# Performance work log

Measured on AMD Instinct MI355X. Metric: run time of the kernel, lower is better.

## Reference

```python
import jax, jax.numpy as jnp
import numpy as np

B, STREAM, IN_CH = 128, 512, 4
EXTRA, GROUPS, DEPTH = 5, 2, 3
STEP, LENGTH = 16, 32
RNN, OUT = 256, 10
C = IN_CH + 1 + EXTRA              # augmented channels: original + time + 1x1-conv
SIG_C = C + C * C + C ** 3          # signature channels per group at depth 3
W = (STREAM - LENGTH) // STEP + 1   # number of sliding windows = GRU steps
F = GROUPS * SIG_C                  # GRU input features


def _outer(a, b):
    # flattened tensor (outer) product on last axis: (...,m),(...,n)->(...,m*n)
    return (a[..., :, None] * b[..., None, :]).reshape(a.shape[:-1] + (a.shape[-1] * b.shape[-1],))


def _chen_step(S, dx):
    # Chen's identity: S <- S (tensor) exp(dx). S is a tuple of flattened
    # signature levels (..., C^k), k=1..DEPTH; dx has shape (..., C).
    P = [jnp.ones(dx.shape[:-1] + (1,), dx.dtype)]  # dx^{(x)j}/j!, j=0..DEPTH
    for j in range(1, DEPTH + 1):
        P.append(_outer(P[-1], dx) / j)
    newS = []
    for k in range(1, DEPTH + 1):
        acc = P[k]  # S_0 (x) P_k
        for j in range(k):
            acc = acc + _outer(S[k - 1 - j], P[j])
        newS.append(acc)
    return tuple(newS)


def setup_inputs() -> dict:
    key = jax.random.key(0)
    ks = jax.random.split(key, 10)
    s_aug = 1.0 / np.sqrt(IN_CH)
    s_rnn = 1.0 / np.sqrt(RNN)
    return {
        "x": jax.random.normal(ks[0], (B, STREAM, IN_CH), jnp.float32),
        "W_aug": jax.random.uniform(ks[1], (GROUPS, EXTRA, IN_CH), jnp.float32, -s_aug, s_aug),
        "b_aug": jax.random.uniform(ks[2], (GROUPS, EXTRA), jnp.float32, -s_aug, s_aug),
        "W_ih": jax.random.uniform(ks[3], (3 * RNN, F), jnp.float32, -s_rnn, s_rnn),
        "W_hh": jax.random.uniform(ks[4], (3 * RNN, RNN), jnp.float32, -s_rnn, s_rnn),
        "b_ih": jax.random.uniform(ks[5], (3 * RNN,), jnp.float32, -s_rnn, s_rnn),
        "b_hh": jax.random.uniform(ks[6], (3 * RNN,), jnp.float32, -s_rnn, s_rnn),
        "W_out": jax.random.uniform(ks[7], (OUT, RNN), jnp.float32, -s_rnn, s_rnn),
        "b_out": jax.random.uniform(ks[8], (OUT,), jnp.float32, -s_rnn, s_rnn),
    }


def reference(x, W_aug, b_aug, W_ih, W_hh, b_ih, b_hh, W_out, b_out):
    # (a) linear augmentation per channel group: [original | time | conv1x1(x)]
    t = jnp.linspace(0.0, 1.0, STREAM, dtype=x.dtype)
    t = jnp.broadcast_to(t[None, :, None], (B, STREAM, 1))
    aug = jnp.einsum('bsi,gei->bgse', x, W_aug) + b_aug[None, :, None, :]  # (B,G,S,EXTRA)
    base = jnp.broadcast_to(jnp.concatenate([x, t], -1)[:, None],
                            (B, GROUPS, STREAM, IN_CH + 1))
    xa = jnp.concatenate([base, aug], -1)            # (B,G,S,C)
    xa = xa.reshape(B * GROUPS, STREAM, C)

    # (b) depth-3 signatures over sliding windows via Chen's identity
    dx = xa[:, 1:] - xa[:, :-1]                       # (BG, S-1, C)
    widx = jnp.arange(W)[:, None] * STEP + jnp.arange(LENGTH - 1)[None, :]
    dxw = dx[:, widx]                                 # (BG, W, L-1, C)
    dxw = jnp.moveaxis(dxw, 2, 0)                     # (L-1, BG, W, C)
    S0 = tuple(jnp.zeros((B * GROUPS, W, C ** k), x.dtype) for k in range(1, DEPTH + 1))
    S, _ = jax.lax.scan(lambda S, d: (_chen_step(S, d), None), S0, dxw)
    sig = jnp.concatenate(S, -1)                      # (BG, W, SIG_C)
    sig = sig.reshape(B, GROUPS, W, SIG_C)
    sig = jnp.moveaxis(sig, 2, 0).reshape(W, B, F)    # (W, B, G*SIG_C)

    # (c) GRU over window signatures (torch.nn.GRUCell math, gate order r,z,n)
    def gru(h, xt):
        gi = xt @ W_ih.T + b_ih
        gh = h @ W_hh.T + b_hh
        ir, iz, inn = jnp.split(gi, 3, -1)
        hr, hz, hn = jnp.split(gh, 3, -1)
        r = jax.nn.sigmoid(ir + hr)
        z = jax.nn.sigmoid(iz + hz)
        n = jnp.tanh(inn + r * hn)
        return (1 - z) * n + z * h, None

    h, _ = jax.lax.scan(gru, jnp.zeros((B, RNN), x.dtype), sig)
    return jax.nn.sigmoid(h @ W_out.T + b_out)        # (B, OUT)
```

## Files before the change

kernel.cpp:

```cpp
#include <hip/hip_runtime.h>
#include <hip/hip_bf16.h>
#include <stdint.h>


typedef _Float16 f16;
typedef f16  f16x2 __attribute__((ext_vector_type(2)));
typedef f16  f16x4 __attribute__((ext_vector_type(4)));
typedef f16  f16x8 __attribute__((ext_vector_type(8)));
typedef float f32x2 __attribute__((ext_vector_type(2)));
typedef float f32x4 __attribute__((ext_vector_type(4)));
typedef float f32x8 __attribute__((ext_vector_type(8)));

#define ASYNC16(gp, lp) __builtin_amdgcn_global_load_lds( \
    (const __attribute__((address_space(1))) void*)(gp),  \
    (__attribute__((address_space(3))) void*)(lp), 16, 0, 0)

#define BAR_LDS() do { asm volatile("s_waitcnt lgkmcnt(0)" ::: "memory"); \
                       __builtin_amdgcn_s_barrier();                      \
                       asm volatile("" ::: "memory"); } while (0)

__device__ __forceinline__ float fexp2(float x) {
    float r; asm("v_exp_f32 %0, %1" : "=v"(r) : "v"(x)); return r;
}
__device__ __forceinline__ float frcp(float x) {
    float r; asm("v_rcp_f32 %0, %1" : "=v"(r) : "v"(x)); return r;
}

__global__ __launch_bounds__(256) void prep_kernel(const float* __restrict__ x,
                                                   const float* __restrict__ W_aug,
                                                   const float* __restrict__ Wih,
                                                   const float* __restrict__ Whh,
                                                   f16* __restrict__ sig16,
                                                   f16* __restrict__ wih16,
                                                   f16* __restrict__ whh16,
                                                   uint8_t* __restrict__ whh8) {
    __shared__ float dxs[4][31][10];
    __shared__ f16 srow[4][1112];
    const int tid = threadIdx.x;
    if (blockIdx.x < 840) {
        int c = blockIdx.x * 256 + tid;
        int r = c / 280, kc = (c - r * 280) * 8;
        const float* src = Wih + (size_t)r * 2220 + kc;
        f16x8 o;
        if (kc + 8 <= 2220) {
            float4 v0 = *(const float4*)(src);
            float4 v1 = *(const float4*)(src + 4);
            o[0]=(f16)v0.x; o[1]=(f16)v0.y; o[2]=(f16)v0.z; o[3]=(f16)v0.w;
            o[4]=(f16)v1.x; o[5]=(f16)v1.y; o[6]=(f16)v1.z; o[7]=(f16)v1.w;
        } else {
#pragma unroll
            for (int j = 0; j < 8; j++)
                o[j] = (f16)((kc + j < 2220) ? src[j] : 0.0f);
        }
        *(f16x8*)(wih16 + (size_t)r * 2240 + kc) = o;
        return;
    }
    if (blockIdx.x < 936) {
        int c2 = ((int)blockIdx.x - 840) * 256 + tid;
        int j8 = c2 * 8;
        float w[8];
        {
            float4 v0 = *(const float4*)(Whh + j8);
            float4 v1 = *(const float4*)(Whh + j8 + 4);
            w[0]=v0.x; w[1]=v0.y; w[2]=v0.z; w[3]=v0.w;
            w[4]=v1.x; w[5]=v1.y; w[6]=v1.z; w[7]=v1.w;
        }
        f16x8 o;
#pragma unroll
        for (int j = 0; j < 8; j++) o[j] = (f16)w[j];
        *(f16x8*)(whh16 + j8) = o;
        {
            uint32_t p01 = (uint32_t)__builtin_amdgcn_cvt_pk_fp8_f32(w[0]*16.f, w[1]*16.f, 0, false) & 0xffffu;
            uint32_t p23 = (uint32_t)__builtin_amdgcn_cvt_pk_fp8_f32(w[2]*16.f, w[3]*16.f, 0, false) & 0xffffu;
            uint32_t p45 = (uint32_t)__builtin_amdgcn_cvt_pk_fp8_f32(w[4]*16.f, w[5]*16.f, 0, false) & 0xffffu;
            uint32_t p67 = (uint32_t)__builtin_amdgcn_cvt_pk_fp8_f32(w[6]*16.f, w[7]*16.f, 0, false) & 0xffffu;
            uint2 st = make_uint2(p01 | (p23 << 16), p45 | (p67 << 16));
            *(uint2*)(whh8 + j8) = st;
        }
        return;
    }
    const int sub = tid >> 6, t64 = tid & 63;
    const int cid = ((int)blockIdx.x - 936) * 4 + sub;
    const int w = cid % 31;
    const int bg = cid / 31;
    const int b = bg >> 1, g = bg & 1;
    if (t64 < 31) {
        int s = w * 16 + t64;
        const float4 x0 = *(const float4*)(x + ((size_t)b * 512 + s) * 4);
        const float4 x1 = *(const float4*)(x + ((size_t)b * 512 + s + 1) * 4);
        float d0 = x1.x - x0.x, d1 = x1.y - x0.y, d2 = x1.z - x0.z, d3 = x1.w - x0.w;
        dxs[sub][t64][0] = d0; dxs[sub][t64][1] = d1;
        dxs[sub][t64][2] = d2; dxs[sub][t64][3] = d3;
        dxs[sub][t64][4] = 1.0f / 511.0f;
#pragma unroll
        for (int e = 0; e < 5; e++) {
            const float* wa = W_aug + (g * 5 + e) * 4;
            dxs[sub][t64][5 + e] = d0 * wa[0] + d1 * wa[1] + d2 * wa[2] + d3 * wa[3];
        }
    }
    __syncthreads();
    size_t base = ((size_t)(w * 128 + b)) * 2240 + (size_t)g * 1110;
    if (t64 < 50) {
        int p0 = 2 * t64, p1 = p0 + 1;
        int i0 = p0 / 10, j0 = p0 % 10, j1 = j0 + 1;
        const float* dz  = &dxs[sub][0][0];
        const float* pI  = dz + i0;
        const float* pJ0 = dz + j0;
        const float* pJ1 = dz + j1;
        float s3a[10], s3b[10];
#pragma unroll
        for (int k = 0; k < 10; k++) { s3a[k] = 0.f; s3b[k] = 0.f; }
        float s2a = 0.f, s2b = 0.f, s1 = 0.f;
        for (int l = 0; l < 31; l++) {
            const float* row = dz + l * 10;
            float di  = pI[l * 10];
            float dj0 = pJ0[l * 10];
            float dj1 = pJ1[l * 10];
            float t0 = s1 + di * (1.0f / 3.0f);
            float a0 = s2a + t0 * (0.5f * dj0);
            float a1 = s2b + t0 * (0.5f * dj1);
#pragma unroll
            for (int k = 0; k < 10; k++) {
                float dk = row[k];
                s3a[k] += a0 * dk;
                s3b[k] += a1 * dk;
            }
            float u = s1 + 0.5f * di;
            s2a += u * dj0;
            s2b += u * dj1;
            s1 += di;
        }
        *(f16x2*)&srow[sub][10 + p0] = (f16x2){(f16)s2a, (f16)s2b};
#pragma unroll
        for (int k = 0; k < 5; k++)
            *(f16x2*)&srow[sub][110 + p0 * 10 + 2 * k] =
                (f16x2){(f16)s3a[2 * k], (f16)s3a[2 * k + 1]};
#pragma unroll
        for (int k = 0; k < 5; k++)
            *(f16x2*)&srow[sub][110 + p1 * 10 + 2 * k] =
                (f16x2){(f16)s3b[2 * k], (f16)s3b[2 * k + 1]};
    } else if (t64 < 60) {
        int c = t64 - 50;
        const float* pc = &dxs[sub][0][0] + c;
        float s = 0.f;
        for (int l = 0; l < 31; l++) s += pc[l * 10];
        srow[sub][c] = (f16)s;
    }
    __syncthreads();
    for (int j = t64; j < 555; j += 64)
        *(f16x2*)(sig16 + base + 2 * j) = *(const f16x2*)&srow[sub][2 * j];
    if (g == 1 && t64 < 10)
        *(f16x2*)(sig16 + ((size_t)(w * 128 + b)) * 2240 + 2220 + 2 * t64) =
            (f16x2){(f16)0.0f, (f16)0.0f};
}

__global__ __launch_bounds__(512) void gemm_kernel(const f16* __restrict__ A,
                                                   const f16* __restrict__ Bw,
                                                   const float* __restrict__ bias,
                                                   const float* __restrict__ bhh,
                                                   f16* __restrict__ Cgi) {
    const int lin = blockIdx.x;
    const int nc = lin % 12;
    const int mb = lin / 12;
    const int t = mb >> 1, half = mb & 1;
    __shared__ __align__(16) f16 As[2][3][64 * 32];
    __shared__ __align__(16) f16 Bs[2][3][64 * 32];
    __shared__ __align__(16) float sc[4][16 * 64];
    const int tid = threadIdx.x, lane = tid & 63, wid = tid >> 6;
    const int kh = wid >> 2, w4 = wid & 3;
    const int l16 = lane & 15, quad = lane >> 4;
    const int lrow = lane >> 2, lk = lane & 3;
    const int Nbase = nc * 64;
    const f16* gaA = A  + (size_t)(mb * 64 + w4 * 16 + lrow) * 2240 + kh * 1120 + lk * 8;
    const f16* gbB = Bw + (size_t)(Nbase + w4 * 16 + lrow) * 2240 + kh * 1120 + lk * 8;

#define GISSUE(KT, BUF) do { \
        int _k0 = (KT) * 32; \
        ASYNC16(gaA + _k0, &As[kh][BUF][(w4 * 16) * 32]); \
        ASYNC16(gbB + _k0, &Bs[kh][BUF][(w4 * 16) * 32]); } while (0)

#define GCOMPUTE(BUF) do { \
        f16x8 af, bf[4]; \
        af = *(const f16x8*)&As[kh][BUF][(w4 * 16 + l16) * 32 + quad * 8]; \
        _Pragma("unroll") \
        for (int nt = 0; nt < 4; nt++) \
            bf[nt] = *(const f16x8*)&Bs[kh][BUF][(nt * 16 + l16) * 32 + quad * 8]; \
        _Pragma("unroll") \
        for (int nt = 0; nt < 4; nt++) \
            acc[nt] = __builtin_amdgcn_mfma_f32_16x16x32_f16(af, bf[nt], acc[nt], 0, 0, 0); } while (0)

    f32x4 acc[4];
#pragma unroll
    for (int nt = 0; nt < 4; nt++) acc[nt] = (f32x4){0.f, 0.f, 0.f, 0.f};

    GISSUE(0, 0); GISSUE(1, 1);
    for (int kt = 0; kt < 33; kt++) {
        asm volatile("s_waitcnt vmcnt(2) lgkmcnt(0)\n\ts_barrier" ::: "memory");
        GISSUE(kt + 2, (kt + 2) % 3);
        GCOMPUTE(kt % 3);
    }
    asm volatile("s_waitcnt vmcnt(2) lgkmcnt(0)\n\ts_barrier" ::: "memory");
    GCOMPUTE(0);
    asm volatile("s_waitcnt vmcnt(0) lgkmcnt(0)\n\ts_barrier" ::: "memory");
    GCOMPUTE(1);

    if (kh == 1) {
#pragma unroll
        for (int nt = 0; nt < 4; nt++)
#pragma unroll
            for (int rr = 0; rr < 4; rr++)
                sc[w4][(quad * 4 + rr) * 64 + nt * 16 + l16] = acc[nt][rr];
    }
    __syncthreads();
    if (kh == 0) {
        const float NEG_LOG2E = -1.4426950408889634f;
        const float TWO_LOG2E =  2.8853900817779268f;
        const int bbv = half * 4 + w4;
#pragma unroll
        for (int nt = 0; nt < 4; nt++) {
            int col = Nbase + nt * 16 + l16;
            float bvv = bias[col] + (col < 512 ? bhh[col] : 0.0f);
            float scl = (col < 512) ? NEG_LOG2E : TWO_LOG2E;
            int gs = col >> 8, hcc = col & 255;
            int gw = hcc >> 5, gtc = (hcc >> 4) & 1, gl = hcc & 15;
            int u = gs * 2 + gtc;
            int gtid = gw * 64 + quad * 16 + gl;
            size_t off = ((size_t)((t * 8 + bbv) * 6 + u)) * 2048 + (size_t)gtid * 4;
            f16x4 st;
#pragma unroll
            for (int rr = 0; rr < 4; rr++) {
                float v = acc[nt][rr] + sc[w4][(quad * 4 + rr) * 64 + nt * 16 + l16];
                st[rr] = (f16)((v + bvv) * scl);
            }
            *(f16x4*)(Cgi + off) = st;
        }
    }
#undef GISSUE
#undef GCOMPUTE
}

#define ACLOB96 \
  "a0","a1","a2","a3","a4","a5","a6","a7","a8","a9","a10","a11","a12","a13","a14","a15", \
  "a16","a17","a18","a19","a20","a21","a22","a23","a24","a25","a26","a27","a28","a29","a30","a31", \
  "a32","a33","a34","a35","a36","a37","a38","a39","a40","a41","a42","a43","a44","a45","a46","a47", \
  "a48","a49","a50","a51","a52","a53","a54","a55","a56","a57","a58","a59","a60","a61","a62","a63", \
  "a64","a65","a66","a67","a68","a69","a70","a71","a72","a73","a74","a75","a76","a77","a78","a79", \
  "a80","a81","a82","a83","a84","a85","a86","a87","a88","a89","a90","a91","a92","a93","a94","a95"

#define LF8X(A0,A1,A2,A3,A4,A5,A6,A7, G, TC, KF) do { \
  const uint8_t* _p = whh8 + (size_t)((G) * 256 + wid * 32 + (TC) * 16 + l16) * 256 + (KF) * 128 + quad * 32; \
  f32x4 _t0 = *(const f32x4*)_p; \
  f32x4 _t1 = *(const f32x4*)(_p + 16); \
  asm volatile("v_accvgpr_write_b32 a" #A0 ", %0\n\t" \
               "v_accvgpr_write_b32 a" #A1 ", %1\n\t" \
               "v_accvgpr_write_b32 a" #A2 ", %2\n\t" \
               "v_accvgpr_write_b32 a" #A3 ", %3\n\t" \
               "v_accvgpr_write_b32 a" #A4 ", %4\n\t" \
               "v_accvgpr_write_b32 a" #A5 ", %5\n\t" \
               "v_accvgpr_write_b32 a" #A6 ", %6\n\t" \
               "v_accvgpr_write_b32 a" #A7 ", %7" \
               :: "v"(_t0[0]), "v"(_t0[1]), "v"(_t0[2]), "v"(_t0[3]), \
                  "v"(_t1[0]), "v"(_t1[1]), "v"(_t1[2]), "v"(_t1[3]) \
               : "a" #A0, "a" #A1, "a" #A2, "a" #A3, \
                 "a" #A4, "a" #A5, "a" #A6, "a" #A7); } while (0)

__global__ __launch_bounds__(512, 2) void gru_kernel(const f16* __restrict__ gi,
                                                     const f16* __restrict__ whh16,
                                                     const uint8_t* __restrict__ whh8,
                                                     const float* __restrict__ b_hh,
                                                     const float* __restrict__ W_out,
                                                     const float* __restrict__ b_out,
                                                     float* __restrict__ out) {
    __shared__ __align__(16) f16 hbufF[16 * 280];
    __shared__ __align__(16) uint8_t hbuf8[2][16 * 272];
    const int tid = threadIdx.x, lane = tid & 63, wid = tid >> 6;
    const int quad = lane >> 4, l16 = lane & 15;
    const int bb = blockIdx.x;

    for (int i = tid; i < 16 * 272; i += 512) hbuf8[1][i] = 0;

    LF8X(0,1,2,3,4,5,6,7,         0,0,0);
    LF8X(8,9,10,11,12,13,14,15,   0,0,1);
    LF8X(16,17,18,19,20,21,22,23, 0,1,0);
    LF8X(24,25,26,27,28,29,30,31, 0,1,1);
    LF8X(32,33,34,35,36,37,38,39, 1,0,0);
    LF8X(40,41,42,43,44,45,46,47, 1,0,1);
    LF8X(48,49,50,51,52,53,54,55, 1,1,0);
    LF8X(56,57,58,59,60,61,62,63, 1,1,1);
    LF8X(64,65,66,67,68,69,70,71, 2,0,0);
    LF8X(72,73,74,75,76,77,78,79, 2,0,1);
    LF8X(80,81,82,83,84,85,86,87, 2,1,0);
    LF8X(88,89,90,91,92,93,94,95, 2,1,1);

    const float C2 = 2.8853900817779268f;
    float bhn[2];
#pragma unroll
    for (int tc = 0; tc < 2; tc++) bhn[tc] = C2 * b_hh[512 + wid * 32 + tc * 16 + l16];
    float hm[2][4];
#pragma unroll
    for (int tc = 0; tc < 2; tc++)
#pragma unroll
        for (int rr = 0; rr < 4; rr++) hm[tc][rr] = 0.f;

    const size_t lanebase = (size_t)bb * 12288 + (size_t)tid * 4;
    f16x4 gcur[6];
#pragma unroll
    for (int u = 0; u < 6; u++)
        gcur[u] = *(const f16x4*)(gi + lanebase + u * 2048);

    const f32x4 zq = (f32x4){0.f, 0.f, 0.f, 0.f};

    BAR_LDS();

    for (int t = 0; t < 31; t++) {
        const uint8_t* hb = ((t & 1) ? hbuf8[0] : hbuf8[1]) + (size_t)l16 * 272 + quad * 32;
        f32x4 aR0, aR1, aZ0, aZ1, aN0, aN1;
        f32x4 u0 = *(const f32x4*)(hb);
        f32x4 u1 = *(const f32x4*)(hb + 16);
        f32x4 u2 = *(const f32x4*)(hb + 128);
        f32x4 u3 = *(const f32x4*)(hb + 144);
        f32x8 A0f, A1f;
        A0f[0]=u0[0]; A0f[1]=u0[1]; A0f[2]=u0[2]; A0f[3]=u0[3];
        A0f[4]=u1[0]; A0f[5]=u1[1]; A0f[6]=u1[2]; A0f[7]=u1[3];
        A1f[0]=u2[0]; A1f[1]=u2[1]; A1f[2]=u2[2]; A1f[3]=u2[3];
        A1f[4]=u3[0]; A1f[5]=u3[1]; A1f[6]=u3[2]; A1f[7]=u3[3];
        __builtin_amdgcn_s_setprio(1);
        asm volatile(
            "v_mfma_f32_16x16x128_f8f6f4 %[r0], %[A0], a[0:7],   %[zq]\n\t"
            "v_mfma_f32_16x16x128_f8f6f4 %[r1], %[A0], a[16:23], %[zq]\n\t"
            "v_mfma_f32_16x16x128_f8f6f4 %[z0], %[A0], a[32:39], %[zq]\n\t"
            "v_mfma_f32_16x16x128_f8f6f4 %[z1], %[A0], a[48:55], %[zq]\n\t"
            "v_mfma_f32_16x16x128_f8f6f4 %[n0], %[A0], a[64:71], %[zq]\n\t"
            "v_mfma_f32_16x16x128_f8f6f4 %[n1], %[A0], a[80:87], %[zq]\n\t"
            "v_mfma_f32_16x16x128_f8f6f4 %[r0], %[A1], a[8:15],  %[r0]\n\t"
            "v_mfma_f32_16x16x128_f8f6f4 %[r1], %[A1], a[24:31], %[r1]\n\t"
            "v_mfma_f32_16x16x128_f8f6f4 %[z0], %[A1], a[40:47], %[z0]\n\t"
            "v_mfma_f32_16x16x128_f8f6f4 %[z1], %[A1], a[56:63], %[z1]\n\t"
            "v_mfma_f32_16x16x128_f8f6f4 %[n0], %[A1], a[72:79], %[n0]\n\t"
            "v_mfma_f32_16x16x128_f8f6f4 %[n1], %[A1], a[88:95], %[n1]\n\t"
            "s_nop 7\n\ts_nop 7"
            : [r0]"=&v"(aR0), [r1]"=&v"(aR1), [z0]"=&v"(aZ0), [z1]"=&v"(aZ1),
              [n0]"=&v"(aN0), [n1]"=&v"(aN1)
            : [A0]"v"(A0f), [A1]"v"(A1f), [zq]"v"(zq)
            : ACLOB96);
        __builtin_amdgcn_s_setprio(0);

        uint8_t* hd8 = hbuf8[t & 1];
        const float C1N16 = -0.09016844005556021f;
        const float C2_16 =  0.18033688011112042f;
#pragma unroll
        for (int tc = 0; tc < 2; tc++) {
            const int hcx = wid * 32 + tc * 16 + l16;
            const f32x4 vR = tc ? aR1 : aR0;
            const f32x4 vZ = tc ? aZ1 : aZ0;
            const f32x4 vN = tc ? aN1 : aN0;
#pragma unroll
            for (int rr = 0; rr < 4; rr++) {
                float rg = frcp(1.f + fexp2(fmaf(C1N16, vR[rr], (float)gcur[tc][rr])));
                float zg = frcp(1.f + fexp2(fmaf(C1N16, vZ[rr], (float)gcur[2 + tc][rr])));
                float t2 = fmaf(rg, fmaf(C2_16, vN[rr], bhn[tc]), (float)gcur[4 + tc][rr]);
                float e2 = fexp2(t2);
                float ng = fmaf(-2.f, frcp(e2 + 1.f), 1.f);
                float h  = fmaf(zg, hm[tc][rr] - ng, ng);
                hm[tc][rr] = h;
                int pk = __builtin_amdgcn_cvt_pk_fp8_f32(h, h, 0, false);
                hd8[(quad * 4 + rr) * 272 + hcx] = (uint8_t)pk;
                if (t == 30)
                    hbufF[(quad * 4 + rr) * 280 + hcx] = (f16)h;
            }
        }
        {
            int tn = (t < 30) ? t + 1 : 30;
            const f16* gsrc = gi + (size_t)tn * 98304 + lanebase;
#pragma unroll
            for (int u = 0; u < 6; u++)
                gcur[u] = *(const f16x4*)(gsrc + u * 2048);
        }
        BAR_LDS();
    }
    if (tid < 160) {
        int r = tid / 10, oc = tid - r * 10;
        const f16* hfin = hbufF;
        float s = b_out[oc];
        for (int k = 0; k < 256; k++) s += (float)hfin[r * 280 + k] * W_out[oc * 256 + k];
        out[(bb * 16 + r) * 10 + oc] = frcp(1.f + __expf(-s));
    }
}

extern "C" void kernel_launch(void* const* d_in, const int* in_sizes, int n_in,
                              void* d_out, int out_size, void* d_ws, size_t ws_size,
                              hipStream_t stream) {
    const float* x     = (const float*)d_in[0];
    const float* W_aug = (const float*)d_in[1];
    const float* W_ih  = (const float*)d_in[3];
    const float* W_hh  = (const float*)d_in[4];
    const float* b_ih  = (const float*)d_in[5];
    const float* b_hh  = (const float*)d_in[6];
    const float* W_out = (const float*)d_in[7];
    const float* b_out = (const float*)d_in[8];
    float* out = (float*)d_out;

    char* ws = (char*)d_ws;
    const size_t SIG_BYTES  = (size_t)3968 * 2240 * 2;
    const size_t WIH_BYTES  = (size_t)768 * 2240 * 2;
    const size_t WHH_BYTES  = (size_t)768 * 256 * 2;
    const size_t WHH8_BYTES = (size_t)768 * 256;
    const size_t GI_BYTES   = (size_t)31 * 8 * 6 * 512 * 4 * 2;
    if (ws_size < SIG_BYTES + WIH_BYTES + WHH_BYTES + WHH8_BYTES + GI_BYTES) return;
    f16* sig16    = (f16*)ws;
    f16* wih16    = (f16*)(ws + SIG_BYTES);
    f16* whh16    = (f16*)(ws + SIG_BYTES + WIH_BYTES);
    uint8_t* whh8 = (uint8_t*)(ws + SIG_BYTES + WIH_BYTES + WHH_BYTES);
    f16* giw      = (f16*)(ws + SIG_BYTES + WIH_BYTES + WHH_BYTES + WHH8_BYTES);

    hipLaunchKernelGGL(prep_kernel, dim3(2920), dim3(256), 0, stream,
                       x, W_aug, W_ih, W_hh, sig16, wih16, whh16, whh8);
    hipLaunchKernelGGL(gemm_kernel, dim3(744), dim3(512), 0, stream,
                       sig16, wih16, b_ih, b_hh, giw);
    hipLaunchKernelGGL(gru_kernel, dim3(8), dim3(512), 0, stream,
                       giw, whh16, whh8, b_hh, W_out, b_out, out);
}
```

Baseline: 177.3 us.

## Split GRU hidden columns across 16 waves per block to shorten per-step chain

New measurement: 176.2 us, median of 2. Within noise of the previous version (-0.6%).

```diff
diff --git a/kernel.cpp b/kernel.cpp
--- a/kernel.cpp
+++ b/kernel.cpp
@@ -239,16 +239,13 @@
 #undef GCOMPUTE
 }
 
-#define ACLOB96 \
+#define ACLOB48 \
   "a0","a1","a2","a3","a4","a5","a6","a7","a8","a9","a10","a11","a12","a13","a14","a15", \
   "a16","a17","a18","a19","a20","a21","a22","a23","a24","a25","a26","a27","a28","a29","a30","a31", \
-  "a32","a33","a34","a35","a36","a37","a38","a39","a40","a41","a42","a43","a44","a45","a46","a47", \
-  "a48","a49","a50","a51","a52","a53","a54","a55","a56","a57","a58","a59","a60","a61","a62","a63", \
-  "a64","a65","a66","a67","a68","a69","a70","a71","a72","a73","a74","a75","a76","a77","a78","a79", \
-  "a80","a81","a82","a83","a84","a85","a86","a87","a88","a89","a90","a91","a92","a93","a94","a95"
-
-#define LF8X(A0,A1,A2,A3,A4,A5,A6,A7, G, TC, KF) do { \
-  const uint8_t* _p = whh8 + (size_t)((G) * 256 + wid * 32 + (TC) * 16 + l16) * 256 + (KF) * 128 + quad * 32; \
+  "a32","a33","a34","a35","a36","a37","a38","a39","a40","a41","a42","a43","a44","a45","a46","a47"
+
+#define LF8X(A0,A1,A2,A3,A4,A5,A6,A7, G, KF) do { \
+  const uint8_t* _p = whh8 + (size_t)((G) * 256 + wid * 16 + l16) * 256 + (KF) * 128 + quad * 32; \
   f32x4 _t0 = *(const f32x4*)_p; \
   f32x4 _t1 = *(const f32x4*)(_p + 16); \
   asm volatile("v_accvgpr_write_b32 a" #A0 ", %0\n\t" \
@@ -264,49 +261,41 @@
                : "a" #A0, "a" #A1, "a" #A2, "a" #A3, \
                  "a" #A4, "a" #A5, "a" #A6, "a" #A7); } while (0)
 
-__global__ __launch_bounds__(512, 2) void gru_kernel(const f16* __restrict__ gi,
-                                                     const f16* __restrict__ whh16,
-                                                     const uint8_t* __restrict__ whh8,
-                                                     const float* __restrict__ b_hh,
-                                                     const float* __restrict__ W_out,
-                                                     const float* __restrict__ b_out,
-                                                     float* __restrict__ out) {
+__global__ __launch_bounds__(1024, 4) void gru_kernel(const f16* __restrict__ gi,
+                                                      const f16* __restrict__ whh16,
+                                                      const uint8_t* __restrict__ whh8,
+                                                      const float* __restrict__ b_hh,
+                                                      const float* __restrict__ W_out,
+                                                      const float* __restrict__ b_out,
+                                                      float* __restrict__ out) {
     __shared__ __align__(16) f16 hbufF[16 * 280];
     __shared__ __align__(16) uint8_t hbuf8[2][16 * 272];
     const int tid = threadIdx.x, lane = tid & 63, wid = tid >> 6;
     const int quad = lane >> 4, l16 = lane & 15;
     const int bb = blockIdx.x;
 
-    for (int i = tid; i < 16 * 272; i += 512) hbuf8[1][i] = 0;
-
-    LF8X(0,1,2,3,4,5,6,7,         0,0,0);
-    LF8X(8,9,10,11,12,13,14,15,   0,0,1);
-    LF8X(16,17,18,19,20,21,22,23, 0,1,0);
-    LF8X(24,25,26,27,28,29,30,31, 0,1,1);
-    LF8X(32,33,34,35,36,37,38,39, 1,0,0);
-    LF8X(40,41,42,43,44,45,46,47, 1,0,1);
-    LF8X(48,49,50,51,52,53,54,55, 1,1,0);
-    LF8X(56,57,58,59,60,61,62,63, 1,1,1);
-    LF8X(64,65,66,67,68,69,70,71, 2,0,0);
-    LF8X(72,73,74,75,76,77,78,79, 2,0,1);
-    LF8X(80,81,82,83,84,85,86,87, 2,1,0);
-    LF8X(88,89,90,91,92,93,94,95, 2,1,1);
+    for (int i = tid; i < 16 * 272; i += 1024) hbuf8[1][i] = 0;
+
+    LF8X(0,1,2,3,4,5,6,7,         0, 0);
+    LF8X(8,9,10,11,12,13,14,15,   0, 1);
+    LF8X(16,17,18,19,20,21,22,23, 1, 0);
+    LF8X(24,25,26,27,28,29,30,31, 1, 1);
+    LF8X(32,33,34,35,36,37,38,39, 2, 0);
+    LF8X(40,41,42,43,44,45,46,47, 2, 1);
 
     const float C2 = 2.8853900817779268f;
-    float bhn[2];
-#pragma unroll
-    for (int tc = 0; tc < 2; tc++) bhn[tc] = C2 * b_hh[512 + wid * 32 + tc * 16 + l16];
-    float hm[2][4];
-#pragma unroll
-    for (int tc = 0; tc < 2; tc++)
-#pragma unroll
-        for (int rr = 0; rr < 4; rr++) hm[tc][rr] = 0.f;
-
-    const size_t lanebase = (size_t)bb * 12288 + (size_t)tid * 4;
-    f16x4 gcur[6];
-#pragma unroll
-    for (int u = 0; u < 6; u++)
-        gcur[u] = *(const f16x4*)(gi + lanebase + u * 2048);
+    const int hcx = wid * 16 + l16;
+    const float bhn = C2 * b_hh[512 + hcx];
+    float hm[4];
+#pragma unroll
+    for (int rr = 0; rr < 4; rr++) hm[rr] = 0.f;
+
+    const size_t lanebase = (size_t)bb * 12288 + (size_t)(wid & 1) * 2048
+                          + (size_t)((wid >> 1) * 64 + quad * 16 + l16) * 4;
+    f16x4 gcur[3];
+#pragma unroll
+    for (int gs = 0; gs < 3; gs++)
+        gcur[gs] = *(const f16x4*)(gi + lanebase + (size_t)gs * 4096);
 
     const f32x4 zq = (f32x4){0.f, 0.f, 0.f, 0.f};
 
@@ -314,7 +303,7 @@
 
     for (int t = 0; t < 31; t++) {
         const uint8_t* hb = ((t & 1) ? hbuf8[0] : hbuf8[1]) + (size_t)l16 * 272 + quad * 32;
-        f32x4 aR0, aR1, aZ0, aZ1, aN0, aN1;
+        f32x4 aR, aZ, aN;
         f32x4 u0 = *(const f32x4*)(hb);
         f32x4 u1 = *(const f32x4*)(hb + 16);
         f32x4 u2 = *(const f32x4*)(hb + 128);
@@ -326,55 +315,41 @@
         A1f[4]=u3[0]; A1f[5]=u3[1]; A1f[6]=u3[2]; A1f[7]=u3[3];
         __builtin_amdgcn_s_setprio(1);
         asm volatile(
-            "v_mfma_f32_16x16x128_f8f6f4 %[r0], %[A0], a[0:7],   %[zq]\n\t"
-            "v_mfma_f32_16x16x128_f8f6f4 %[r1], %[A0], a[16:23], %[zq]\n\t"
-            "v_mfma_f32_16x16x128_f8f6f4 %[z0], %[A0], a[32:39], %[zq]\n\t"
-            "v_mfma_f32_16x16x128_f8f6f4 %[z1], %[A0], a[48:55], %[zq]\n\t"
-            "v_mfma_f32_16x16x128_f8f6f4 %[n0], %[A0], a[64:71], %[zq]\n\t"
-            "v_mfma_f32_16x16x128_f8f6f4 %[n1], %[A0], a[80:87], %[zq]\n\t"
-            "v_mfma_f32_16x16x128_f8f6f4 %[r0], %[A1], a[8:15],  %[r0]\n\t"
-            "v_mfma_f32_16x16x128_f8f6f4 %[r1], %[A1], a[24:31], %[r1]\n\t"
-            "v_mfma_f32_16x16x128_f8f6f4 %[z0], %[A1], a[40:47], %[z0]\n\t"
-            "v_mfma_f32_16x16x128_f8f6f4 %[z1], %[A1], a[56:63], %[z1]\n\t"
-            "v_mfma_f32_16x16x128_f8f6f4 %[n0], %[A1], a[72:79], %[n0]\n\t"
-            "v_mfma_f32_16x16x128_f8f6f4 %[n1], %[A1], a[88:95], %[n1]\n\t"
+            "v_mfma_f32_16x16x128_f8f6f4 %[r], %[A0], a[0:7],   %[zq]\n\t"
+            "v_mfma_f32_16x16x128_f8f6f4 %[z], %[A0], a[16:23], %[zq]\n\t"
+            "v_mfma_f32_16x16x128_f8f6f4 %[n], %[A0], a[32:39], %[zq]\n\t"
+            "v_mfma_f32_16x16x128_f8f6f4 %[r], %[A1], a[8:15],  %[r]\n\t"
+            "v_mfma_f32_16x16x128_f8f6f4 %[z], %[A1], a[24:31], %[z]\n\t"
+            "v_mfma_f32_16x16x128_f8f6f4 %[n], %[A1], a[40:47], %[n]\n\t"
             "s_nop 7\n\ts_nop 7"
-            : [r0]"=&v"(aR0), [r1]"=&v"(aR1), [z0]"=&v"(aZ0), [z1]"=&v"(aZ1),
-              [n0]"=&v"(aN0), [n1]"=&v"(aN1)
+            : [r]"=&v"(aR), [z]"=&v"(aZ), [n]"=&v"(aN)
             : [A0]"v"(A0f), [A1]"v"(A1f), [zq]"v"(zq)
-            : ACLOB96);
+            : ACLOB48);
         __builtin_amdgcn_s_setprio(0);
 
         uint8_t* hd8 = hbuf8[t & 1];
         const float C1N16 = -0.09016844005556021f;
         const float C2_16 =  0.18033688011112042f;
 #pragma unroll
-        for (int tc = 0; tc < 2; tc++) {
-            const int hcx = wid * 32 + tc * 16 + l16;
-            const f32x4 vR = tc ? aR1 : aR0;
-            const f32x4 vZ = tc ? aZ1 : aZ0;
-            const f32x4 vN = tc ? aN1 : aN0;
-#pragma unroll
-            for (int rr = 0; rr < 4; rr++) {
-                float rg = frcp(1.f + fexp2(fmaf(C1N16, vR[rr], (float)gcur[tc][rr])));
-                float zg = frcp(1.f + fexp2(fmaf(C1N16, vZ[rr], (float)gcur[2 + tc][rr])));
-                float t2 = fmaf(rg, fmaf(C2_16, vN[rr], bhn[tc]), (float)gcur[4 + tc][rr]);
-                float e2 = fexp2(t2);
-                float ng = fmaf(-2.f, frcp(e2 + 1.f), 1.f);
-                float h  = fmaf(zg, hm[tc][rr] - ng, ng);
-                hm[tc][rr] = h;
-                int pk = __builtin_amdgcn_cvt_pk_fp8_f32(h, h, 0, false);
-                hd8[(quad * 4 + rr) * 272 + hcx] = (uint8_t)pk;
-                if (t == 30)
-                    hbufF[(quad * 4 + rr) * 280 + hcx] = (f16)h;
-            }
+        for (int rr = 0; rr < 4; rr++) {
+            float rg = frcp(1.f + fexp2(fmaf(C1N16, aR[rr], (float)gcur[0][rr])));
+            float zg = frcp(1.f + fexp2(fmaf(C1N16, aZ[rr], (float)gcur[1][rr])));
+            float t2 = fmaf(rg, fmaf(C2_16, aN[rr], bhn), (float)gcur[2][rr]);
+            float e2 = fexp2(t2);
+            float ng = fmaf(-2.f, frcp(e2 + 1.f), 1.f);
+            float h  = fmaf(zg, hm[rr] - ng, ng);
+            hm[rr] = h;
+            int pk = __builtin_amdgcn_cvt_pk_fp8_f32(h, h, 0, false);
+            hd8[(quad * 4 + rr) * 272 + hcx] = (uint8_t)pk;
+            if (t == 30)
+                hbufF[(quad * 4 + rr) * 280 + hcx] = (f16)h;
         }
         {
             int tn = (t < 30) ? t + 1 : 30;
             const f16* gsrc = gi + (size_t)tn * 98304 + lanebase;
 #pragma unroll
-            for (int u = 0; u < 6; u++)
-                gcur[u] = *(const f16x4*)(gsrc + u * 2048);
+            for (int gs = 0; gs < 3; gs++)
+                gcur[gs] = *(const f16x4*)(gsrc + (size_t)gs * 4096);
         }
         BAR_LDS();
     }
@@ -417,6 +392,6 @@
                        x, W_aug, W_ih, W_hh, sig16, wih16, whh16, whh8);
     hipLaunchKernelGGL(gemm_kernel, dim3(744), dim3(512), 0, stream,
                        sig16, wih16, b_ih, b_hh, giw);
-    hipLaunchKernelGGL(gru_kernel, dim3(8), dim3(512), 0, stream,
+    hipLaunchKernelGGL(gru_kernel, dim3(8), dim3(1024), 0, stream,
                        giw, whh16, whh8, b_hh, W_out, b_out, out);
 }
```
